# Kernel optimization log

Measured on AMD Instinct MI355X. Metric: run time of the kernel, lower is better.

## Reference

```python
import jax, jax.numpy as jnp
import numpy as np
from math import sqrt

B, Q, S, D, H = 2, 2048, 2048, 1024, 16
ADIM = D // H
IEPS = 1e-32


def setup_inputs() -> dict:
    key = jax.random.key(0)
    ks = jax.random.split(key, 7)
    sc = 0.02
    return {
        "iQ": jax.random.normal(ks[0], (B, Q, D), jnp.float32),
        "iK": jax.random.normal(ks[1], (B, S, D), jnp.float32),
        "mask": jax.random.randint(ks[2], (B, Q, S), 0, 2) > 0,
        "Wq": jax.random.normal(ks[3], (D, D), jnp.float32) * sc,
        "Wkv": jax.random.normal(ks[4], (2 * D, D), jnp.float32) * sc,
        "Wo": jax.random.normal(ks[5], (D, D), jnp.float32) * sc,
        "nbias": jnp.zeros((1,), jnp.float32),
    }


def sparse_norm(scores, nbias):
    # ReLU(x + b)^2 normalized along last axis (SparseNormer)
    t = jax.nn.relu(scores + nbias[0])
    t = t * t
    return t / (t.sum(-1, keepdims=True) + IEPS)


def reference(iQ, iK, mask, Wq, Wkv, Wo, nbias):
    b, q, _ = iQ.shape
    s = iK.shape[1]
    # projections (no bias)
    rq = (iQ @ Wq.T).reshape(b, q, H, ADIM)            # bqhd
    kv = (iK @ Wkv.T).reshape(b, s, 2, H, ADIM)
    rk, rv = kv[:, :, 0], kv[:, :, 1]                  # bshd each
    scores = jnp.einsum("bqhd,bshd->bhqs", rq, rk) / sqrt(ADIM)
    scores = jnp.where(mask[:, None, :, :], jnp.float32(-1e32), scores)
    attn = sparse_norm(scores, nbias)
    o = jnp.einsum("bhqs,bshd->bqhd", attn, rv).reshape(b, q, H * ADIM)
    return o @ Wo.T
```

## Files before the change

### kernel.cpp

```cpp
#include <hip/hip_runtime.h>

#define Bb 2
#define Qq 2048
#define Ss 2048
#define Dd 1024
#define Hh 16
#define AD 64

typedef __attribute__((ext_vector_type(8))) short bf16x8;
typedef __attribute__((ext_vector_type(4))) short bf16x4;
typedef __attribute__((ext_vector_type(4))) float f32x4;
typedef unsigned short u16;
typedef unsigned int u32;
typedef unsigned long long u64;

__device__ __forceinline__ u16 f2bf(float f) {
  union { float f; u32 u; } v; v.f = f;
  u32 r = v.u + 0x7fffu + ((v.u >> 16) & 1u);
  return (u16)(r >> 16);
}

__device__ __forceinline__ void gld16(const u16* g, u16* l) {
  __builtin_amdgcn_global_load_lds(
      (const __attribute__((address_space(1))) unsigned int*)g,
      (__attribute__((address_space(3))) unsigned int*)l, 16, 0, 0);
}

__global__ __launch_bounds__(256) void cast_all_k(const float* __restrict__ iQ,
                                                  const float* __restrict__ iK,
                                                  const float* __restrict__ Wq,
                                                  const float* __restrict__ Wkv,
                                                  const float* __restrict__ Wo,
                                                  u16* __restrict__ Qb, u16* __restrict__ Kb,
                                                  u16* __restrict__ Wqb, u16* __restrict__ Wkvb,
                                                  u16* __restrict__ Wob) {
  int i = blockIdx.x * 256 + threadIdx.x;
  const float* src; u16* dst; int off;
  if (i < 1048576)      { src = iQ;  dst = Qb;   off = 0; }
  else if (i < 2097152) { src = iK;  dst = Kb;   off = 1048576; }
  else if (i < 2359296) { src = Wq;  dst = Wqb;  off = 2097152; }
  else if (i < 2883584) { src = Wkv; dst = Wkvb; off = 2359296; }
  else                  { src = Wo;  dst = Wob;  off = 2883584; }
  int j = i - off;
  float4 v = ((const float4*)src)[j];
  ushort4 o;
  o.x = f2bf(v.x); o.y = f2bf(v.y); o.z = f2bf(v.z); o.w = f2bf(v.w);
  ((ushort4*)dst)[j] = o;
}

__global__ __launch_bounds__(256) void maskpack_k(const int* __restrict__ mask,
                                                  u64* __restrict__ mb64) {
  int flat = blockIdx.x * 256 + threadIdx.x;
  int st = flat & 31;
  int q  = (flat >> 5) & 2047;
  int b  = flat >> 16;
  const int4* src = (const int4*)(mask + ((size_t)(b * Qq + q)) * Ss + st * 64);
  u64 bits = 0;
#pragma unroll
  for (int c = 0; c < 16; c++) {
    int4 v = src[c];
    bits |= (u64)(v.x != 0) << (c * 4 + 0);
    bits |= (u64)(v.y != 0) << (c * 4 + 1);
    bits |= (u64)(v.z != 0) << (c * 4 + 2);
    bits |= (u64)(v.w != 0) << (c * 4 + 3);
  }
  mb64[flat] = bits;
}

__global__ __launch_bounds__(256) void vtrans_k(const u16* __restrict__ KV,
                                                u16* __restrict__ VT) {
  __shared__ u16 T[64 * 72];
  const int tid = threadIdx.x;
  const int s0 = blockIdx.x * 64, h = blockIdx.y, b = blockIdx.z;
#pragma unroll
  for (int c = tid; c < 512; c += 256) {
    int row = c >> 3, col8 = (c & 7) * 8;
    *(int4*)(T + row * 72 + col8) =
        *(const int4*)(KV + ((size_t)(b * Ss + s0 + row)) * (2 * Dd) + Dd + h * AD + col8);
  }
  __syncthreads();
#pragma unroll
  for (int c = tid; c < 512; c += 256) {
    int drow = c >> 3, s8 = (c & 7) * 8;
    u16 tmp[8];
#pragma unroll
    for (int j = 0; j < 8; j++) tmp[j] = T[(s8 + j) * 72 + drow];
    *(int4*)(VT + (((size_t)(b * Hh + h)) * AD + drow) * Ss + s0 + s8) = *(int4*)tmp;
  }
}

template <int WRITE_F32>
__global__ __launch_bounds__(256) void gemm_bt(const u16* __restrict__ A,
                                               const u16* __restrict__ W,
                                               void* __restrict__ C,
                                               int M, int N, int K) {
  __shared__ u16 As[128 * 32];
  __shared__ u16 Ws[64 * 32];
  const int tid = threadIdx.x;
  const int lane = tid & 63, wave = tid >> 6;
  const int qr = lane & 15, quad = lane >> 4;
  const int m0 = blockIdx.x * 128, n0 = blockIdx.y * 64;
  const int wm = (wave >> 1) * 64, wn = (wave & 1) * 32;
  f32x4 acc[4][2] = {};
  const int sr = tid >> 2;
  const int sc = tid & 3;
  const u16* arow1 = A + (size_t)(m0 + sr) * K;
  const u16* arow2 = A + (size_t)(m0 + sr + 64) * K;
  const u16* wrow1 = W + (size_t)(n0 + sr) * K;
  const int gc1 = (sc ^ ((sr >> 1) & 3)) * 8;
  const int gc2 = (sc ^ (((sr + 64) >> 1) & 3)) * 8;
  u16* ld_a1 = As + sr * 32 + sc * 8;
  u16* ld_a2 = As + (sr + 64) * 32 + sc * 8;
  u16* ld_w1 = Ws + sr * 32 + sc * 8;

  for (int k0 = 0; k0 < K; k0 += 32) {
    gld16(arow1 + k0 + gc1, ld_a1);
    gld16(arow2 + k0 + gc2, ld_a2);
    gld16(wrow1 + k0 + gc1, ld_w1);
    __syncthreads();
    bf16x8 af[4], bw[2];
#pragma unroll
    for (int i = 0; i < 4; i++) {
      int row = wm + i * 16 + qr;
      af[i] = *(const bf16x8*)(As + row * 32 + (quad ^ ((row >> 1) & 3)) * 8);
    }
#pragma unroll
    for (int j = 0; j < 2; j++) {
      int row = wn + j * 16 + qr;
      bw[j] = *(const bf16x8*)(Ws + row * 32 + (quad ^ ((row >> 1) & 3)) * 8);
    }
#pragma unroll
    for (int i = 0; i < 4; i++)
#pragma unroll
      for (int j = 0; j < 2; j++)
        acc[i][j] = __builtin_amdgcn_mfma_f32_16x16x32_bf16(af[i], bw[j], acc[i][j], 0, 0, 0);
    __syncthreads();
  }
#pragma unroll
  for (int i = 0; i < 4; i++)
#pragma unroll
    for (int j = 0; j < 2; j++)
#pragma unroll
      for (int r = 0; r < 4; r++) {
        int row = m0 + wm + i * 16 + quad * 4 + r;
        int col = n0 + wn + j * 16 + qr;
        float v = acc[i][j][r];
        if (WRITE_F32) ((float*)C)[(size_t)row * N + col] = v;
        else           ((u16*)C)[(size_t)row * N + col] = f2bf(v);
      }
}

__global__ __launch_bounds__(512, 4) void attn_k(const u16* __restrict__ RQ,
                                                 const u16* __restrict__ KV,
                                                 const u16* __restrict__ VT,
                                                 const u64* __restrict__ mb64,
                                                 const float* __restrict__ nbias,
                                                 u16* __restrict__ O) {
  __shared__ char LB[33792];
  u16* Ks    = (u16*)LB;
  u16* Vts   = (u16*)(LB + 16384);
  float* denS = (float*)(LB + 32768);
  f32x4* Xch = (f32x4*)LB;

  const int tid = threadIdx.x, lane = tid & 63, w = tid >> 6;
  const int qh = w >> 1, sh = w & 1;
  const int qr = lane & 15, quad = lane >> 4;
  const int q0 = blockIdx.x * 128, h = blockIdx.y, b = blockIdx.z;
  const u16* rqb = RQ + ((size_t)(b * Qq + q0)) * Dd + h * AD;
  const u16* kb  = KV + ((size_t)b * Ss) * (2 * Dd) + h * AD;
  const u16* vtb = VT + ((size_t)(b * Hh + h)) * AD * Ss;
  const u64* mbase = mb64 + ((size_t)(b * Qq + q0)) * 32;
  const float nb = nbias[0];

  bf16x8 bq[2][2];
#pragma unroll
  for (int j = 0; j < 2; j++)
#pragma unroll
    for (int kk = 0; kk < 2; kk++)
      bq[j][kk] = *(const bf16x8*)(rqb + (size_t)(qh * 32 + j * 16 + qr) * Dd +
                                   kk * 32 + quad * 8);

  f32x4 acc[2][4] = {};
  float den[2] = {0.f, 0.f};

  const int krS = tid >> 3, kcS = tid & 7;
  const int vrS = tid >> 4, vcS = tid & 15;

  for (int t = 0; t < 16; t++) {
    __syncthreads();
    const int s0 = t * 128;
#pragma unroll
    for (int is = 0; is < 2; is++) {
      int row = is * 64 + krS;
      gld16(kb + (size_t)(s0 + row) * (2 * Dd) + ((kcS ^ (row & 7)) * 8),
            Ks + row * 64 + kcS * 8);
    }
#pragma unroll
    for (int is = 0; is < 2; is++) {
      int row = is * 32 + vrS;
      gld16(vtb + (size_t)row * Ss + s0 + ((vcS ^ (row & 7)) * 8),
            Vts + row * 128 + vcS * 8);
    }
    u64 mw[2];
#pragma unroll
    for (int j = 0; j < 2; j++)
      mw[j] = mbase[(size_t)(qh * 32 + j * 16 + qr) * 32 + (t << 1) + sh];
    __syncthreads();

#pragma unroll
    for (int mi = 0; mi < 4; mi++) {
      int krow = sh * 64 + mi * 16 + qr;
      const u16* kbase = Ks + krow * 64;
      bf16x8 ak0 = *(const bf16x8*)(kbase + ((quad)     ^ (krow & 7)) * 8);
      bf16x8 ak1 = *(const bf16x8*)(kbase + ((quad + 4) ^ (krow & 7)) * 8);
      f32x4 asc[2] = {};
#pragma unroll
      for (int j = 0; j < 2; j++) {
        asc[j] = __builtin_amdgcn_mfma_f32_16x16x32_bf16(ak0, bq[j][0], asc[j], 0, 0, 0);
        asc[j] = __builtin_amdgcn_mfma_f32_16x16x32_bf16(ak1, bq[j][1], asc[j], 0, 0, 0);
      }
      union { u32 w2[2]; bf16x4 v; } pk[2];
#pragma unroll
      for (int j = 0; j < 2; j++) {
        u32 mm = (u32)(mw[j] >> (mi * 16 + quad * 4)) & 0xFu;
        u32 th[4];
#pragma unroll
        for (int r = 0; r < 4; r++) {
          float v = __builtin_fmaf(asc[j][r], 0.125f, nb);
          float tt = fmaxf(v, 0.f);
          tt = tt * tt;
          if ((mm >> r) & 1) tt = 0.f;
          union { float f; u32 u; } cv; cv.f = tt;
          th[r] = cv.u & 0xffff0000u;
          union { u32 u; float f; } tv; tv.u = th[r];
          den[j] += tv.f;
        }
        pk[j].w2[0] = (th[0] >> 16) | th[1];
        pk[j].w2[1] = (th[2] >> 16) | th[3];
      }
      int g = sh * 16 + mi * 4 + quad;
#pragma unroll
      for (int nn = 0; nn < 4; nn++) {
        int vrow = nn * 16 + qr;
        bf16x4 bv = *(const bf16x4*)(Vts + vrow * 128 + (g ^ ((vrow & 7) << 1)) * 4);
#pragma unroll
        for (int j = 0; j < 2; j++)
          acc[j][nn] = __builtin_amdgcn_mfma_f32_16x16x16bf16_1k(pk[j].v, bv, acc[j][nn], 0, 0, 0);
      }
    }
  }

  __syncthreads();

#pragma unroll
  for (int j = 0; j < 2; j++) {
    den[j] += __shfl_xor(den[j], 16, 64);
    den[j] += __shfl_xor(den[j], 32, 64);
  }
  if (quad == 0) {
#pragma unroll
    for (int j = 0; j < 2; j++)
      denS[sh * 128 + qh * 32 + j * 16 + qr] = den[j];
  }
  if (sh == 1) {
#pragma unroll
    for (int j = 0; j < 2; j++)
#pragma unroll
      for (int nn = 0; nn < 4; nn++)
        Xch[qh * 512 + (j * 4 + nn) * 64 + lane] = acc[j][nn];
  }
  __syncthreads();

  if (sh == 0) {
    u16* ob = O + ((size_t)(b * Qq + q0)) * Dd + h * AD;
#pragma unroll
    for (int j = 0; j < 2; j++) {
      float rc[4];
#pragma unroll
      for (int r = 0; r < 4; r++) {
        int ql = qh * 32 + j * 16 + quad * 4 + r;
        rc[r] = 1.f / (denS[ql] + denS[128 + ql] + 1e-32f);
      }
#pragma unroll
      for (int nn = 0; nn < 4; nn++) {
        f32x4 s4 = acc[j][nn];
        f32x4 p4 = Xch[qh * 512 + (j * 4 + nn) * 64 + lane];
#pragma unroll
        for (int r = 0; r < 4; r++) {
          int ql = qh * 32 + j * 16 + quad * 4 + r;
          ob[(size_t)ql * Dd + nn * 16 + qr] = f2bf((s4[r] + p4[r]) * rc[r]);
        }
      }
    }
  }
}

extern "C" void kernel_launch(void* const* d_in, const int* in_sizes, int n_in,
                              void* d_out, int out_size, void* d_ws, size_t ws_size,
                              hipStream_t stream) {
  const float* iQ   = (const float*)d_in[0];
  const float* iK   = (const float*)d_in[1];
  const int*   mask = (const int*)d_in[2];
  const float* Wq   = (const float*)d_in[3];
  const float* Wkv  = (const float*)d_in[4];
  const float* Wo   = (const float*)d_in[5];
  const float* nb   = (const float*)d_in[6];

  char* ws = (char*)d_ws;
  u16* Qb   = (u16*)(ws + (size_t)0);
  u16* Kb   = (u16*)(ws + ((size_t)8  << 20));
  u16* Wqb  = (u16*)(ws + ((size_t)16 << 20));
  u16* Wkvb = (u16*)(ws + ((size_t)18 << 20));
  u16* Wob  = (u16*)(ws + ((size_t)22 << 20));
  u16* RQ   = (u16*)(ws + ((size_t)24 << 20));
  u16* KV   = (u16*)(ws + ((size_t)32 << 20));
  u16* Obuf = (u16*)(ws + ((size_t)48 << 20));
  u16* VT   = (u16*)(ws + ((size_t)56 << 20));
  u64* MB   = (u64*)(ws + ((size_t)64 << 20));

  cast_all_k<<<12288, 256, 0, stream>>>(iQ, iK, Wq, Wkv, Wo, Qb, Kb, Wqb, Wkvb, Wob);
  maskpack_k<<<512, 256, 0, stream>>>(mask, MB);

  gemm_bt<0><<<dim3(32, 16), 256, 0, stream>>>(Qb, Wqb, RQ, 4096, 1024, 1024);
  gemm_bt<0><<<dim3(32, 32), 256, 0, stream>>>(Kb, Wkvb, KV, 4096, 2048, 1024);
  vtrans_k<<<dim3(32, 16, 2), 256, 0, stream>>>(KV, VT);

  attn_k<<<dim3(16, 16, 2), 512, 0, stream>>>(RQ, KV, VT, MB, nb, Obuf);

  gemm_bt<1><<<dim3(32, 16), 256, 0, stream>>>(Obuf, Wob, d_out, 4096, 1024, 1024);
}
```

Measured before the change: 267.4 us.

## Fuse Q/KV projections with V transpose, widen tiles, move denominator to MFMA

Merges the Q and KV projection GEMMs into one launch whose V-half blocks write the transposed V directly, which removes the separate vtrans kernel and a launch. GEMM K-tiles double to 64 with an 8-way XOR swizzle. The 1/sqrt(d) scale is folded into the Q projection, and nbias is used as the initial accumulator value. Attention now stages 256-key tiles, packs to bf16 with v_perm, and computes the row denominator with an MFMA against a ones vector instead of scalar adds and shuffles. The changes target launch overhead, LDS synchronisation count and VALU work, at the cost of more LDS per block, which may reduce occupancy; the denominator is now summed from rounded bf16 values by the MFMA.

```diff
diff --git a/kernel.cpp b/kernel.cpp
--- a/kernel.cpp
+++ b/kernel.cpp
@@ -6,6 +6,7 @@
 #define Dd 1024
 #define Hh 16
 #define AD 64
+#define KK 1024
 
 typedef __attribute__((ext_vector_type(8))) short bf16x8;
 typedef __attribute__((ext_vector_type(4))) short bf16x4;
@@ -67,73 +68,168 @@
   mb64[flat] = bits;
 }
 
-__global__ __launch_bounds__(256) void vtrans_k(const u16* __restrict__ KV,
-                                                u16* __restrict__ VT) {
-  __shared__ u16 T[64 * 72];
-  const int tid = threadIdx.x;
-  const int s0 = blockIdx.x * 64, h = blockIdx.y, b = blockIdx.z;
-#pragma unroll
-  for (int c = tid; c < 512; c += 256) {
-    int row = c >> 3, col8 = (c & 7) * 8;
-    *(int4*)(T + row * 72 + col8) =
-        *(const int4*)(KV + ((size_t)(b * Ss + s0 + row)) * (2 * Dd) + Dd + h * AD + col8);
-  }
-  __syncthreads();
-#pragma unroll
-  for (int c = tid; c < 512; c += 256) {
-    int drow = c >> 3, s8 = (c & 7) * 8;
-    u16 tmp[8];
-#pragma unroll
-    for (int j = 0; j < 8; j++) tmp[j] = T[(s8 + j) * 72 + drow];
-    *(int4*)(VT + (((size_t)(b * Hh + h)) * AD + drow) * Ss + s0 + s8) = *(int4*)tmp;
-  }
-}
-
-template <int WRITE_F32>
-__global__ __launch_bounds__(256) void gemm_bt(const u16* __restrict__ A,
-                                               const u16* __restrict__ W,
-                                               void* __restrict__ C,
-                                               int M, int N, int K) {
-  __shared__ u16 As[128 * 32];
-  __shared__ u16 Ws[64 * 32];
+__global__ __launch_bounds__(256, 4) void proj_k(const u16* __restrict__ Qb,
+                                                 const u16* __restrict__ Kb,
+                                                 const u16* __restrict__ Wqb,
+                                                 const u16* __restrict__ Wkvb,
+                                                 u16* __restrict__ RQ,
+                                                 u16* __restrict__ KV,
+                                                 u16* __restrict__ VT) {
+  __shared__ u16 LDS[128 * 64 + 64 * 64];
+  u16* As = LDS;
+  u16* Ws = LDS + 128 * 64;
+  u16* Tt = LDS;
   const int tid = threadIdx.x;
   const int lane = tid & 63, wave = tid >> 6;
   const int qr = lane & 15, quad = lane >> 4;
-  const int m0 = blockIdx.x * 128, n0 = blockIdx.y * 64;
+  const int bid = blockIdx.x;
+  const bool isQ = bid < 512;
+  const int b2 = isQ ? bid : bid - 512;
+  const int m0 = (b2 & 31) * 128;
+  const int n0 = (b2 >> 5) * 64;
+  const u16* A = isQ ? Qb : Kb;
+  const u16* W = isQ ? Wqb : Wkvb;
   const int wm = (wave >> 1) * 64, wn = (wave & 1) * 32;
+  const int qs = qr & 7;
+
+  const int sr = tid >> 3, sc = tid & 7;
+  const u16 *aP[4], *wP[2];
+  u16 *aL[4], *wL[2];
+#pragma unroll
+  for (int is = 0; is < 4; is++) {
+    int row = is * 32 + sr;
+    aP[is] = A + (size_t)(m0 + row) * KK + ((sc ^ (row & 7)) * 8);
+    aL[is] = As + row * 64 + sc * 8;
+  }
+#pragma unroll
+  for (int is = 0; is < 2; is++) {
+    int row = is * 32 + sr;
+    wP[is] = W + (size_t)(n0 + row) * KK + ((sc ^ (row & 7)) * 8);
+    wL[is] = Ws + row * 64 + sc * 8;
+  }
+
   f32x4 acc[4][2] = {};
-  const int sr = tid >> 2;
-  const int sc = tid & 3;
-  const u16* arow1 = A + (size_t)(m0 + sr) * K;
-  const u16* arow2 = A + (size_t)(m0 + sr + 64) * K;
-  const u16* wrow1 = W + (size_t)(n0 + sr) * K;
-  const int gc1 = (sc ^ ((sr >> 1) & 3)) * 8;
-  const int gc2 = (sc ^ (((sr + 64) >> 1) & 3)) * 8;
-  u16* ld_a1 = As + sr * 32 + sc * 8;
-  u16* ld_a2 = As + (sr + 64) * 32 + sc * 8;
-  u16* ld_w1 = Ws + sr * 32 + sc * 8;
-
-  for (int k0 = 0; k0 < K; k0 += 32) {
-    gld16(arow1 + k0 + gc1, ld_a1);
-    gld16(arow2 + k0 + gc2, ld_a2);
-    gld16(wrow1 + k0 + gc1, ld_w1);
-    __syncthreads();
-    bf16x8 af[4], bw[2];
-#pragma unroll
-    for (int i = 0; i < 4; i++) {
-      int row = wm + i * 16 + qr;
-      af[i] = *(const bf16x8*)(As + row * 32 + (quad ^ ((row >> 1) & 3)) * 8);
-    }
-#pragma unroll
-    for (int j = 0; j < 2; j++) {
-      int row = wn + j * 16 + qr;
-      bw[j] = *(const bf16x8*)(Ws + row * 32 + (quad ^ ((row >> 1) & 3)) * 8);
-    }
+
+  for (int k0 = 0; k0 < KK; k0 += 64) {
+#pragma unroll
+    for (int is = 0; is < 4; is++) gld16(aP[is] + k0, aL[is]);
+#pragma unroll
+    for (int is = 0; is < 2; is++) gld16(wP[is] + k0, wL[is]);
+    __syncthreads();
+#pragma unroll
+    for (int kk = 0; kk < 2; kk++) {
+      bf16x8 af[4], bw[2];
+#pragma unroll
+      for (int i = 0; i < 4; i++)
+        af[i] = *(const bf16x8*)(As + (wm + i * 16 + qr) * 64 + (((kk * 4 + quad) ^ qs) * 8));
+#pragma unroll
+      for (int j = 0; j < 2; j++)
+        bw[j] = *(const bf16x8*)(Ws + (wn + j * 16 + qr) * 64 + (((kk * 4 + quad) ^ qs) * 8));
+#pragma unroll
+      for (int i = 0; i < 4; i++)
+#pragma unroll
+        for (int j = 0; j < 2; j++)
+          acc[i][j] = __builtin_amdgcn_mfma_f32_16x16x32_bf16(af[i], bw[j], acc[i][j], 0, 0, 0);
+    }
+    __syncthreads();
+  }
+
+  if (isQ) {
 #pragma unroll
     for (int i = 0; i < 4; i++)
 #pragma unroll
       for (int j = 0; j < 2; j++)
-        acc[i][j] = __builtin_amdgcn_mfma_f32_16x16x32_bf16(af[i], bw[j], acc[i][j], 0, 0, 0);
+#pragma unroll
+        for (int r = 0; r < 4; r++) {
+          int row = m0 + wm + i * 16 + quad * 4 + r;
+          int col = n0 + wn + j * 16 + qr;
+          RQ[(size_t)row * 1024 + col] = f2bf(acc[i][j][r] * 0.125f);
+        }
+  } else if (n0 < 1024) {
+#pragma unroll
+    for (int i = 0; i < 4; i++)
+#pragma unroll
+      for (int j = 0; j < 2; j++)
+#pragma unroll
+        for (int r = 0; r < 4; r++) {
+          int row = m0 + wm + i * 16 + quad * 4 + r;
+          int col = n0 + wn + j * 16 + qr;
+          KV[(size_t)row * 2048 + col] = f2bf(acc[i][j][r]);
+        }
+  } else {
+#pragma unroll
+    for (int i = 0; i < 4; i++)
+#pragma unroll
+      for (int j = 0; j < 2; j++)
+#pragma unroll
+        for (int r = 0; r < 4; r++) {
+          int srow = wm + i * 16 + quad * 4 + r;
+          int d    = wn + j * 16 + qr;
+          Tt[d * 136 + srow] = f2bf(acc[i][j][r]);
+        }
+    __syncthreads();
+    const int h = (n0 - 1024) >> 6;
+    const int bb = m0 >> 11, sbase = m0 & 2047;
+    u16* vdst = VT + (((size_t)(bb * Hh + h)) * AD) * Ss;
+    const int d = tid >> 2;
+#pragma unroll
+    for (int ic = 0; ic < 4; ic++) {
+      int ch = ic * 4 + (tid & 3);
+      *(int4*)(vdst + (size_t)d * Ss + sbase + ch * 8) = *(const int4*)(Tt + d * 136 + ch * 8);
+    }
+  }
+}
+
+__global__ __launch_bounds__(256, 4) void oproj_k(const u16* __restrict__ A,
+                                                  const u16* __restrict__ W,
+                                                  float* __restrict__ C) {
+  __shared__ u16 LDS[128 * 64 + 64 * 64];
+  u16* As = LDS;
+  u16* Ws = LDS + 128 * 64;
+  const int tid = threadIdx.x;
+  const int lane = tid & 63, wave = tid >> 6;
+  const int qr = lane & 15, quad = lane >> 4;
+  const int m0 = (blockIdx.x & 31) * 128;
+  const int n0 = (blockIdx.x >> 5) * 64;
+  const int wm = (wave >> 1) * 64, wn = (wave & 1) * 32;
+  const int qs = qr & 7;
+  const int sr = tid >> 3, sc = tid & 7;
+  const u16 *aP[4], *wP[2];
+  u16 *aL[4], *wL[2];
+#pragma unroll
+  for (int is = 0; is < 4; is++) {
+    int row = is * 32 + sr;
+    aP[is] = A + (size_t)(m0 + row) * KK + ((sc ^ (row & 7)) * 8);
+    aL[is] = As + row * 64 + sc * 8;
+  }
+#pragma unroll
+  for (int is = 0; is < 2; is++) {
+    int row = is * 32 + sr;
+    wP[is] = W + (size_t)(n0 + row) * KK + ((sc ^ (row & 7)) * 8);
+    wL[is] = Ws + row * 64 + sc * 8;
+  }
+  f32x4 acc[4][2] = {};
+  for (int k0 = 0; k0 < KK; k0 += 64) {
+#pragma unroll
+    for (int is = 0; is < 4; is++) gld16(aP[is] + k0, aL[is]);
+#pragma unroll
+    for (int is = 0; is < 2; is++) gld16(wP[is] + k0, wL[is]);
+    __syncthreads();
+#pragma unroll
+    for (int kk = 0; kk < 2; kk++) {
+      bf16x8 af[4], bw[2];
+#pragma unroll
+      for (int i = 0; i < 4; i++)
+        af[i] = *(const bf16x8*)(As + (wm + i * 16 + qr) * 64 + (((kk * 4 + quad) ^ qs) * 8));
+#pragma unroll
+      for (int j = 0; j < 2; j++)
+        bw[j] = *(const bf16x8*)(Ws + (wn + j * 16 + qr) * 64 + (((kk * 4 + quad) ^ qs) * 8));
+#pragma unroll
+      for (int i = 0; i < 4; i++)
+#pragma unroll
+        for (int j = 0; j < 2; j++)
+          acc[i][j] = __builtin_amdgcn_mfma_f32_16x16x32_bf16(af[i], bw[j], acc[i][j], 0, 0, 0);
+    }
     __syncthreads();
   }
 #pragma unroll
@@ -144,9 +240,7 @@
       for (int r = 0; r < 4; r++) {
         int row = m0 + wm + i * 16 + quad * 4 + r;
         int col = n0 + wn + j * 16 + qr;
-        float v = acc[i][j][r];
-        if (WRITE_F32) ((float*)C)[(size_t)row * N + col] = v;
-        else           ((u16*)C)[(size_t)row * N + col] = f2bf(v);
+        C[(size_t)row * 1024 + col] = acc[i][j][r];
       }
 }
 
@@ -156,18 +250,18 @@
                                                  const u64* __restrict__ mb64,
                                                  const float* __restrict__ nbias,
                                                  u16* __restrict__ O) {
-  __shared__ char LB[33792];
-  u16* Ks    = (u16*)LB;
-  u16* Vts   = (u16*)(LB + 16384);
-  float* denS = (float*)(LB + 32768);
+  __shared__ char LB[65536];
+  u16* Ks  = (u16*)LB;
+  u16* Vts = (u16*)(LB + 32768);
   f32x4* Xch = (f32x4*)LB;
 
   const int tid = threadIdx.x, lane = tid & 63, w = tid >> 6;
   const int qh = w >> 1, sh = w & 1;
   const int qr = lane & 15, quad = lane >> 4;
+  const int quad4 = quad * 4, qs = qr & 7;
   const int q0 = blockIdx.x * 128, h = blockIdx.y, b = blockIdx.z;
   const u16* rqb = RQ + ((size_t)(b * Qq + q0)) * Dd + h * AD;
-  const u16* kb  = KV + ((size_t)b * Ss) * (2 * Dd) + h * AD;
+  const u16* kb  = KV + ((size_t)b * Ss) * 2048 + h * AD;
   const u16* vtb = VT + ((size_t)(b * Hh + h)) * AD * Ss;
   const u64* mbase = mb64 + ((size_t)(b * Qq + q0)) * 32;
   const float nb = nbias[0];
@@ -180,115 +274,114 @@
       bq[j][kk] = *(const bf16x8*)(rqb + (size_t)(qh * 32 + j * 16 + qr) * Dd +
                                    kk * 32 + quad * 8);
 
+  const u16 *kP[4], *vP[4];
+  u16 *kL[4], *vL[4];
+  {
+    const int r8 = tid >> 3, c8 = tid & 7;
+#pragma unroll
+    for (int is = 0; is < 4; is++) {
+      int row = is * 64 + r8;
+      kP[is] = kb + (size_t)row * 2048 + ((c8 ^ (row & 7)) * 8);
+      kL[is] = Ks + row * 64 + c8 * 8;
+    }
+    const int r32 = tid >> 5, c32 = tid & 31;
+#pragma unroll
+    for (int is = 0; is < 4; is++) {
+      int row = is * 16 + r32;
+      vP[is] = vtb + (size_t)row * Ss + ((c32 ^ (row & 7)) * 8);
+      vL[is] = Vts + row * 256 + c32 * 8;
+    }
+  }
+
+  const bf16x4 vones = { (short)0x3F80, (short)0x3F80, (short)0x3F80, (short)0x3F80 };
   f32x4 acc[2][4] = {};
-  float den[2] = {0.f, 0.f};
-
-  const int krS = tid >> 3, kcS = tid & 7;
-  const int vrS = tid >> 4, vcS = tid & 15;
-
-  for (int t = 0; t < 16; t++) {
-    __syncthreads();
-    const int s0 = t * 128;
-#pragma unroll
-    for (int is = 0; is < 2; is++) {
-      int row = is * 64 + krS;
-      gld16(kb + (size_t)(s0 + row) * (2 * Dd) + ((kcS ^ (row & 7)) * 8),
-            Ks + row * 64 + kcS * 8);
-    }
-#pragma unroll
-    for (int is = 0; is < 2; is++) {
-      int row = is * 32 + vrS;
-      gld16(vtb + (size_t)row * Ss + s0 + ((vcS ^ (row & 7)) * 8),
-            Vts + row * 128 + vcS * 8);
-    }
-    u64 mw[2];
-#pragma unroll
-    for (int j = 0; j < 2; j++)
-      mw[j] = mbase[(size_t)(qh * 32 + j * 16 + qr) * 32 + (t << 1) + sh];
-    __syncthreads();
-
-#pragma unroll
-    for (int mi = 0; mi < 4; mi++) {
-      int krow = sh * 64 + mi * 16 + qr;
-      const u16* kbase = Ks + krow * 64;
-      bf16x8 ak0 = *(const bf16x8*)(kbase + ((quad)     ^ (krow & 7)) * 8);
-      bf16x8 ak1 = *(const bf16x8*)(kbase + ((quad + 4) ^ (krow & 7)) * 8);
-      f32x4 asc[2] = {};
+  f32x4 accd[2] = {};
+
+  const u16* kfr = Ks + (sh * 128 + qr) * 64;
+  const u16* kfr0 = kfr + ((quad ^ qs) * 8);
+  const u16* kfr1 = kfr + (((quad + 4) ^ qs) * 8);
+
+  for (int t = 0; t < 8; t++) {
+    __syncthreads();
+#pragma unroll
+    for (int is = 0; is < 4; is++) gld16(kP[is] + (size_t)t * 524288, kL[is]);
+#pragma unroll
+    for (int is = 0; is < 4; is++) gld16(vP[is] + t * 256, vL[is]);
+    u64 mw[2][2];
+#pragma unroll
+    for (int j = 0; j < 2; j++) {
+      const u64* mp = mbase + (size_t)(qh * 32 + j * 16 + qr) * 32 + t * 4 + sh * 2;
+      mw[j][0] = mp[0];
+      mw[j][1] = mp[1];
+    }
+    __syncthreads();
+
+#pragma unroll
+    for (int mi = 0; mi < 8; mi++) {
+      bf16x8 ak0 = *(const bf16x8*)(kfr0 + mi * 1024);
+      bf16x8 ak1 = *(const bf16x8*)(kfr1 + mi * 1024);
+      f32x4 asc0 = { nb, nb, nb, nb };
+      f32x4 asc1 = { nb, nb, nb, nb };
+      asc0 = __builtin_amdgcn_mfma_f32_16x16x32_bf16(ak0, bq[0][0], asc0, 0, 0, 0);
+      asc0 = __builtin_amdgcn_mfma_f32_16x16x32_bf16(ak1, bq[0][1], asc0, 0, 0, 0);
+      asc1 = __builtin_amdgcn_mfma_f32_16x16x32_bf16(ak0, bq[1][0], asc1, 0, 0, 0);
+      asc1 = __builtin_amdgcn_mfma_f32_16x16x32_bf16(ak1, bq[1][1], asc1, 0, 0, 0);
+
+      union { u32 w2[2]; bf16x4 v; } pk[2];
 #pragma unroll
       for (int j = 0; j < 2; j++) {
-        asc[j] = __builtin_amdgcn_mfma_f32_16x16x32_bf16(ak0, bq[j][0], asc[j], 0, 0, 0);
-        asc[j] = __builtin_amdgcn_mfma_f32_16x16x32_bf16(ak1, bq[j][1], asc[j], 0, 0, 0);
-      }
-      union { u32 w2[2]; bf16x4 v; } pk[2];
-#pragma unroll
-      for (int j = 0; j < 2; j++) {
-        u32 mm = (u32)(mw[j] >> (mi * 16 + quad * 4)) & 0xFu;
+        f32x4 asc = j ? asc1 : asc0;
+        u32 mm = (u32)(mw[j][mi >> 2] >> ((mi & 3) * 16 + quad4)) & 0xFu;
         u32 th[4];
 #pragma unroll
         for (int r = 0; r < 4; r++) {
-          float v = __builtin_fmaf(asc[j][r], 0.125f, nb);
-          float tt = fmaxf(v, 0.f);
+          float tt = fmaxf(asc[r], 0.f);
           tt = tt * tt;
           if ((mm >> r) & 1) tt = 0.f;
           union { float f; u32 u; } cv; cv.f = tt;
-          th[r] = cv.u & 0xffff0000u;
-          union { u32 u; float f; } tv; tv.u = th[r];
-          den[j] += tv.f;
+          th[r] = cv.u;
         }
-        pk[j].w2[0] = (th[0] >> 16) | th[1];
-        pk[j].w2[1] = (th[2] >> 16) | th[3];
+        pk[j].w2[0] = __builtin_amdgcn_perm(th[1], th[0], 0x07060302u);
+        pk[j].w2[1] = __builtin_amdgcn_perm(th[3], th[2], 0x07060302u);
+        accd[j] = __builtin_amdgcn_mfma_f32_16x16x16bf16_1k(pk[j].v, vones, accd[j], 0, 0, 0);
       }
-      int g = sh * 16 + mi * 4 + quad;
+      int g = ((sh * 32 + mi * 4 + quad) ^ (qs << 1)) * 4;
 #pragma unroll
       for (int nn = 0; nn < 4; nn++) {
-        int vrow = nn * 16 + qr;
-        bf16x4 bv = *(const bf16x4*)(Vts + vrow * 128 + (g ^ ((vrow & 7) << 1)) * 4);
-#pragma unroll
-        for (int j = 0; j < 2; j++)
-          acc[j][nn] = __builtin_amdgcn_mfma_f32_16x16x16bf16_1k(pk[j].v, bv, acc[j][nn], 0, 0, 0);
+        bf16x4 bv = *(const bf16x4*)(Vts + (nn * 16 + qr) * 256 + g);
+        acc[0][nn] = __builtin_amdgcn_mfma_f32_16x16x16bf16_1k(pk[0].v, bv, acc[0][nn], 0, 0, 0);
+        acc[1][nn] = __builtin_amdgcn_mfma_f32_16x16x16bf16_1k(pk[1].v, bv, acc[1][nn], 0, 0, 0);
       }
     }
   }
 
   __syncthreads();
-
-#pragma unroll
-  for (int j = 0; j < 2; j++) {
-    den[j] += __shfl_xor(den[j], 16, 64);
-    den[j] += __shfl_xor(den[j], 32, 64);
-  }
-  if (quad == 0) {
-#pragma unroll
-    for (int j = 0; j < 2; j++)
-      denS[sh * 128 + qh * 32 + j * 16 + qr] = den[j];
-  }
   if (sh == 1) {
 #pragma unroll
-    for (int j = 0; j < 2; j++)
+    for (int j = 0; j < 2; j++) {
 #pragma unroll
       for (int nn = 0; nn < 4; nn++)
-        Xch[qh * 512 + (j * 4 + nn) * 64 + lane] = acc[j][nn];
+        Xch[qh * 640 + (j * 4 + nn) * 64 + lane] = acc[j][nn];
+      Xch[qh * 640 + (8 + j) * 64 + lane] = accd[j];
+    }
   }
   __syncthreads();
-
   if (sh == 0) {
     u16* ob = O + ((size_t)(b * Qq + q0)) * Dd + h * AD;
 #pragma unroll
     for (int j = 0; j < 2; j++) {
+      f32x4 dpart = Xch[qh * 640 + (8 + j) * 64 + lane];
       float rc[4];
 #pragma unroll
-      for (int r = 0; r < 4; r++) {
-        int ql = qh * 32 + j * 16 + quad * 4 + r;
-        rc[r] = 1.f / (denS[ql] + denS[128 + ql] + 1e-32f);
-      }
+      for (int r = 0; r < 4; r++)
+        rc[r] = 1.f / (accd[j][r] + dpart[r] + 1e-32f);
 #pragma unroll
       for (int nn = 0; nn < 4; nn++) {
-        f32x4 s4 = acc[j][nn];
-        f32x4 p4 = Xch[qh * 512 + (j * 4 + nn) * 64 + lane];
+        f32x4 p4 = Xch[qh * 640 + (j * 4 + nn) * 64 + lane];
 #pragma unroll
         for (int r = 0; r < 4; r++) {
           int ql = qh * 32 + j * 16 + quad * 4 + r;
-          ob[(size_t)ql * Dd + nn * 16 + qr] = f2bf((s4[r] + p4[r]) * rc[r]);
+          ob[(size_t)ql * Dd + nn * 16 + qr] = f2bf((acc[j][nn][r] + p4[r]) * rc[r]);
         }
       }
     }
@@ -321,11 +414,9 @@
   cast_all_k<<<12288, 256, 0, stream>>>(iQ, iK, Wq, Wkv, Wo, Qb, Kb, Wqb, Wkvb, Wob);
   maskpack_k<<<512, 256, 0, stream>>>(mask, MB);
 
-  gemm_bt<0><<<dim3(32, 16), 256, 0, stream>>>(Qb, Wqb, RQ, 4096, 1024, 1024);
-  gemm_bt<0><<<dim3(32, 32), 256, 0, stream>>>(Kb, Wkvb, KV, 4096, 2048, 1024);
-  vtrans_k<<<dim3(32, 16, 2), 256, 0, stream>>>(KV, VT);
+  proj_k<<<1536, 256, 0, stream>>>(Qb, Kb, Wqb, Wkvb, RQ, KV, VT);
 
   attn_k<<<dim3(16, 16, 2), 512, 0, stream>>>(RQ, KV, VT, MB, nb, Obuf);
 
-  gemm_bt<1><<<dim3(32, 16), 256, 0, stream>>>(Obuf, Wob, d_out, 4096, 1024, 1024);
-}
+  oproj_k<<<512, 256, 0, stream>>>(Obuf, Wob, (float*)d_out);
+}
```

Result: faster. 229.3 us (-14.2%).
